# Kernel tuning notes

Measured on AMD Instinct MI355X. Metric: run time of the kernel, lower is better.

The kernel has to match this reference:

```python
import jax, jax.numpy as jnp
import numpy as np

NEG = -1e12


def setup_inputs() -> dict:
    key = jax.random.key(0)
    ks = jax.random.split(key, 6)
    B, S, D, H = 32, 2048, 1024, 1024  # batch, seq, dec/enc dim, hidden
    last_state = jax.random.normal(ks[0], (B, D), dtype=jnp.float32)
    enc_outputs = jax.random.normal(ks[1], (B, S, D), dtype=jnp.float32)
    attn_masks = jax.random.randint(ks[2], (B, S), 0, 2, dtype=jnp.int32)
    W = jax.random.normal(ks[3], (H, 2 * D), dtype=jnp.float32) * 0.02
    b = jax.random.normal(ks[4], (H,), dtype=jnp.float32) * 0.02
    V = jax.random.normal(ks[5], (H,), dtype=jnp.float32)
    return {"last_state": last_state, "enc_outputs": enc_outputs,
            "attn_masks": attn_masks, "W": W, "b": b, "V": V}


def reference(last_state, enc_outputs, attn_masks, W, b, V):
    # Split W to avoid materializing the [B,S,2D] concat:
    # concat([h, e]) @ W.T == h @ Wh.T + e @ We.T
    D = last_state.shape[-1]
    Wh, We = W[:, :D], W[:, D:]
    # hidden part: [B,H], broadcast over seq
    h_part = jnp.einsum('bd,hd->bh', last_state, Wh)  # [B,H]
    e_part = jnp.einsum('bsd,hd->bsh', enc_outputs, We)  # [B,S,H]
    sim = jnp.tanh(h_part[:, None, :] + e_part + b)  # [B,S,H]
    scores = jnp.einsum('bsh,h->bs', sim, V)  # [B,S]
    scores = jnp.where(attn_masks != 1, jnp.float32(NEG), scores)
    attn_weights = jax.nn.softmax(scores, axis=1)  # [B,S]
    context = jnp.einsum('bs,bsd->bd', attn_weights, enc_outputs)  # [B,D]
    return context, attn_weights, scores
```

## Files before the change

### kernel.cpp

```cpp
#include <hip/hip_runtime.h>
#include <math.h>
#include <stdint.h>

#define B_ 32
#define S_ 2048
#define D_ 1024
#define H_ 1024
#define NEGV -1000000000000.0f

typedef __attribute__((ext_vector_type(8))) short bf16x8;
typedef __attribute__((ext_vector_type(8))) _Float16 f16x8;
typedef __attribute__((ext_vector_type(4))) float f32x4;

static __device__ __forceinline__ unsigned short f2bf(float x) {
    union { float f; unsigned u; } v; v.f = x;
    unsigned r = v.u + 0x7FFF + ((v.u >> 16) & 1);
    return (unsigned short)(r >> 16);
}
static __device__ __forceinline__ float bf2f(unsigned short h) {
    union { float f; unsigned u; } v; v.u = ((unsigned)h) << 16; return v.f;
}
static __device__ __forceinline__ unsigned short f2h(float x) {
    _Float16 h = (_Float16)x; unsigned short u;
    __builtin_memcpy(&u, &h, 2); return u;
}
static __device__ __forceinline__ float h2f(unsigned short u) {
    _Float16 h; __builtin_memcpy(&h, &u, 2); return (float)h;
}
static __device__ __forceinline__ float tanh_fast(float x) {
    float e = __expf(2.f * x);
    return 1.f - 2.f / (e + 1.f);
}
static __device__ __forceinline__ void gl_lds16(unsigned short* lds, const unsigned short* g) {
    __builtin_amdgcn_global_load_lds(
        (const __attribute__((address_space(1))) unsigned int*)(const void*)g,
        (__attribute__((address_space(3))) unsigned int*)(void*)lds,
        16, 0, 0);
}

__global__ __launch_bounds__(256) void k_W_f16(const float* __restrict__ W,
                                               unsigned short* __restrict__ out) {
    int idx = blockIdx.x * 256 + threadIdx.x;
    int h = idx >> 7, kc = idx & 127;
    const float* src = W + (size_t)h * (2 * D_) + D_ + kc * 8;
    float4 a = *(const float4*)src;
    float4 c4 = *(const float4*)(src + 4);
    float v[8] = {a.x, a.y, a.z, a.w, c4.x, c4.y, c4.z, c4.w};
    unsigned short t[8];
#pragma unroll
    for (int j = 0; j < 8; ++j) t[j] = f2h(v[j]);
    uint4 w;
    w.x = t[0] | ((unsigned)t[1] << 16); w.y = t[2] | ((unsigned)t[3] << 16);
    w.z = t[4] | ((unsigned)t[5] << 16); w.w = t[6] | ((unsigned)t[7] << 16);
    int g = kc >> 3, cc = kc & 7;
    int dst = g * 64 + ((cc ^ (h & 7)) << 3);
    *(uint4*)(out + (size_t)h * D_ + dst) = w;
}

__global__ __launch_bounds__(256) void k_hpart(const float* __restrict__ ls,
                                               const float* __restrict__ W,
                                               float* __restrict__ hp) {
    int bh = blockIdx.x * 256 + threadIdx.x;
    int b = bh >> 10, h = bh & 1023;
    const float* lsr = ls + b * D_;
    const float* wr  = W + (size_t)h * (2 * D_);
    float acc = 0.f;
#pragma unroll 4
    for (int d = 0; d < D_; d += 4) {
        float4 a = *(const float4*)(lsr + d);
        float4 w = *(const float4*)(wr + d);
        acc += a.x * w.x + a.y * w.y + a.z * w.z + a.w * w.w;
    }
    hp[bh] = acc;
}

__global__ __launch_bounds__(512, 2) void k_scores_fused(
    const float* __restrict__ enc,
    const unsigned short* __restrict__ Wf16,
    const float* __restrict__ hp, const float* __restrict__ bias,
    const float* __restrict__ V, float* __restrict__ spart)
{
    extern __shared__ unsigned short smem[];
    unsigned short* smemA = smem;
    unsigned short* smemB = smem + 16384;

    const int tid  = threadIdx.x;
    const int lane = tid & 63, wid = tid >> 6;
    const int wm = wid >> 2, wn = wid & 3;
    const int l15 = lane & 15, lhi = lane >> 4;

    const int bid  = blockIdx.x;
    const int wgid = (bid & 7) * 128 + (bid >> 3);
    const int mt = wgid >> 2, nt = wgid & 3;
    const int m0 = mt * 256;
    const int nt256 = nt * 256;
    const int b = m0 >> 11;

    const size_t boff = (size_t)(nt256 + wid * 16 + (lane >> 3)) * D_ + (lane & 7) * 8;
    const int ldsw = wid * 1024;

    f32x4 acc[8][4];
#pragma unroll
    for (int i = 0; i < 8; ++i)
#pragma unroll
        for (int j = 0; j < 4; ++j)
            acc[i][j] = (f32x4){0.f, 0.f, 0.f, 0.f};

    const int swz = l15 & 7;

    float4 ar0[4], ar1[4];

#define LOAD_A(KOFS) do {                                                           \
    _Pragma("unroll")                                                               \
    for (int s_ = 0; s_ < 4; ++s_) {                                                \
        int p_ = tid + s_ * 512;                                                    \
        int row_ = p_ >> 3, pc_ = p_ & 7;                                           \
        const float* ap_ = enc + (size_t)(m0 + row_) * D_ + (KOFS) + pc_ * 8;       \
        ar0[s_] = *(const float4*)ap_;                                              \
        ar1[s_] = *(const float4*)(ap_ + 4);                                        \
    }                                                                               \
} while (0)
#define WRITE_A() do {                                                              \
    _Pragma("unroll")                                                               \
    for (int s_ = 0; s_ < 4; ++s_) {                                                \
        int p_ = tid + s_ * 512;                                                    \
        int row_ = p_ >> 3, pc_ = p_ & 7;                                           \
        float v_[8] = {ar0[s_].x, ar0[s_].y, ar0[s_].z, ar0[s_].w,                  \
                       ar1[s_].x, ar1[s_].y, ar1[s_].z, ar1[s_].w};                 \
        unsigned short t_[8];                                                       \
        _Pragma("unroll")                                                           \
        for (int j_ = 0; j_ < 8; ++j_) t_[j_] = f2h(v_[j_]);                        \
        uint4 w_;                                                                   \
        w_.x = t_[0] | ((unsigned)t_[1] << 16); w_.y = t_[2] | ((unsigned)t_[3] << 16); \
        w_.z = t_[4] | ((unsigned)t_[5] << 16); w_.w = t_[6] | ((unsigned)t_[7] << 16); \
        *(uint4*)&smemA[row_ * 64 + ((pc_ ^ (row_ & 7)) << 3)] = w_;                \
    }                                                                               \
} while (0)

#define STAGE_B(HALF, KOFS) do {                                                    \
    unsigned short* d_ = &smemB[(HALF) * 8192 + ldsw];                              \
    const unsigned short* s_ = Wf16 + boff + (size_t)(HALF) * 131072 + (KOFS);      \
    gl_lds16(d_, s_);                                                               \
    gl_lds16(d_ + 512, s_ + 8192);                                                  \
} while (0)

#define LDA(AR, MH, KS) do {                                                        \
    _Pragma("unroll")                                                               \
    for (int fi_ = 0; fi_ < 4; ++fi_) {                                             \
        int row_ = wm * 128 + (MH) * 64 + fi_ * 16 + l15;                           \
        int ch_  = ((KS) * 4 + lhi) ^ swz;                                          \
        AR[fi_] = *(const f16x8*)&smemA[row_ * 64 + ch_ * 8];                       \
    }                                                                               \
} while (0)
#define LDB(BR, KS) do {                                                            \
    _Pragma("unroll")                                                               \
    for (int fi_ = 0; fi_ < 4; ++fi_) {                                             \
        int row_ = wn * 64 + fi_ * 16 + l15;                                        \
        int ch_  = ((KS) * 4 + lhi) ^ swz;                                          \
        BR[fi_] = *(const f16x8*)&smemB[row_ * 64 + ch_ * 8];                       \
    }                                                                               \
} while (0)
#define MFMA16(AR, BR, MH) do {                                                     \
    _Pragma("unroll")                                                               \
    for (int fi_ = 0; fi_ < 4; ++fi_)                                               \
    _Pragma("unroll")                                                               \
        for (int fj_ = 0; fj_ < 4; ++fj_)                                           \
            acc[(MH) * 4 + fi_][fj_] = __builtin_amdgcn_mfma_f32_16x16x32_f16(      \
                AR[fi_], BR[fj_], acc[(MH) * 4 + fi_][fj_], 0, 0, 0);               \
} while (0)

    LOAD_A(0);
    WRITE_A();
    STAGE_B(0, 0);
    STAGE_B(1, 0);
    __syncthreads();

    f16x8 a[4], bk[4];
#pragma unroll 1
    for (int t = 0; t < 16; ++t) {
        const int kofs = (t + 1) * 64;

        if (t < 15) LOAD_A(kofs);

#pragma unroll
        for (int ks = 0; ks < 2; ++ks) {
            LDB(bk, ks);
            LDA(a, 0, ks);
            MFMA16(a, bk, 0);
            LDA(a, 1, ks);
            MFMA16(a, bk, 1);
        }

        __syncthreads();

        if (t < 15) {
            WRITE_A();
            STAGE_B(0, kofs);
            STAGE_B(1, kofs);
        }

        __syncthreads();
    }

    float hb[4], vv[4];
#pragma unroll
    for (int fn = 0; fn < 4; ++fn) {
        int h = nt256 + wn * 64 + fn * 16 + l15;
        hb[fn] = hp[b * H_ + h] + bias[h];
        vv[fn] = V[h];
    }
    float* s_red = (float*)smem;
#pragma unroll
    for (int fm = 0; fm < 8; ++fm)
#pragma unroll
        for (int rg = 0; rg < 4; ++rg) {
            float rs = 0.f;
#pragma unroll
            for (int fn = 0; fn < 4; ++fn)
                rs += tanh_fast(acc[fm][fn][rg] + hb[fn]) * vv[fn];
            rs += __shfl_xor(rs, 1, 16);
            rs += __shfl_xor(rs, 2, 16);
            rs += __shfl_xor(rs, 4, 16);
            rs += __shfl_xor(rs, 8, 16);
            if (l15 == 0)
                s_red[wid * 128 + fm * 16 + lhi * 4 + rg] = rs;
        }
    __syncthreads();
    if (tid < 256) {
        int wmr = tid >> 7, rr = tid & 127;
        float v = s_red[(wmr * 4 + 0) * 128 + rr] + s_red[(wmr * 4 + 1) * 128 + rr]
                + s_red[(wmr * 4 + 2) * 128 + rr] + s_red[(wmr * 4 + 3) * 128 + rr];
        spart[(size_t)nt * 65536 + m0 + tid] = v;
    }
#undef LOAD_A
#undef WRITE_A
#undef STAGE_B
#undef LDA
#undef LDB
#undef MFMA16
}

__global__ __launch_bounds__(256) void k_softmax_fold(const float* __restrict__ spart,
                                                      const int* __restrict__ mask,
                                                      float* __restrict__ scores_out,
                                                      float* __restrict__ weights) {
    __shared__ float red[8];
    int b = blockIdx.x, tid = threadIdx.x;
    float vals[8];
    float mx = -INFINITY;
#pragma unroll
    for (int i = 0; i < 8; ++i) {
        int m = b * S_ + tid + i * 256;
        float s = spart[m] + spart[65536 + m] + spart[131072 + m] + spart[196608 + m];
        s = (mask[m] == 1) ? s : NEGV;
        scores_out[m] = s;
        vals[i] = s;
        mx = fmaxf(mx, s);
    }
    for (int off = 32; off; off >>= 1) mx = fmaxf(mx, __shfl_xor(mx, off, 64));
    int wave = tid >> 6;
    if ((tid & 63) == 0) red[wave] = mx;
    __syncthreads();
    mx = fmaxf(fmaxf(red[0], red[1]), fmaxf(red[2], red[3]));
    float sum = 0.f;
#pragma unroll
    for (int i = 0; i < 8; ++i) {
        vals[i] = expf(vals[i] - mx);
        sum += vals[i];
    }
    for (int off = 32; off; off >>= 1) sum += __shfl_xor(sum, off, 64);
    if ((tid & 63) == 0) red[4 + wave] = sum;
    __syncthreads();
    sum = red[4] + red[5] + red[6] + red[7];
    float inv = 1.f / sum;
#pragma unroll
    for (int i = 0; i < 8; ++i)
        weights[b * S_ + tid + i * 256] = vals[i] * inv;
}

__global__ __launch_bounds__(256) void k_ctx_partial_f32(const float* __restrict__ weights,
                                                         const float* __restrict__ enc,
                                                         float* __restrict__ part) {
    int b = blockIdx.x >> 4;
    int chunk = blockIdx.x & 15;
    int tid = threadIdx.x;
    int d0 = tid * 4;
    float4 acc = {0.f, 0.f, 0.f, 0.f};
    int s0 = chunk * 128;
    const float* wrow = weights + b * S_;
    for (int s = s0; s < s0 + 128; ++s) {
        float w = wrow[s];
        if (w != 0.f) {
            float4 e = *(const float4*)(enc + (size_t)(b * S_ + s) * D_ + d0);
            acc.x += w * e.x; acc.y += w * e.y; acc.z += w * e.z; acc.w += w * e.w;
        }
    }
    *(float4*)(part + (size_t)blockIdx.x * D_ + d0) = acc;
}

__global__ __launch_bounds__(256) void k_ctx_reduce(const float* __restrict__ part,
                                                    float* __restrict__ ctx) {
    int bd = blockIdx.x * 256 + threadIdx.x;
    int b = bd >> 10, d = bd & 1023;
    float acc = 0.f;
#pragma unroll
    for (int c = 0; c < 16; ++c)
        acc += part[(size_t)(b * 16 + c) * D_ + d];
    ctx[bd] = acc;
}

__global__ __launch_bounds__(256) void k_splitW_lin(const float* __restrict__ W,
                                                    unsigned short* __restrict__ hi,
                                                    unsigned short* __restrict__ lo) {
    int idx = blockIdx.x * 256 + threadIdx.x;
    int h = idx >> 7, kc = idx & 127;
    const float* src = W + (size_t)h * (2 * D_) + D_ + kc * 8;
    float4 a = *(const float4*)src;
    float4 c = *(const float4*)(src + 4);
    float v[8] = {a.x, a.y, a.z, a.w, c.x, c.y, c.z, c.w};
    unsigned short th[8], tl[8];
#pragma unroll
    for (int j = 0; j < 8; ++j) {
        th[j] = f2bf(v[j]);
        tl[j] = f2bf(v[j] - bf2f(th[j]));
    }
    uint4 hw, lw;
    hw.x = th[0] | ((unsigned)th[1] << 16); hw.y = th[2] | ((unsigned)th[3] << 16);
    hw.z = th[4] | ((unsigned)th[5] << 16); hw.w = th[6] | ((unsigned)th[7] << 16);
    lw.x = tl[0] | ((unsigned)tl[1] << 16); lw.y = tl[2] | ((unsigned)tl[3] << 16);
    lw.z = tl[4] | ((unsigned)tl[5] << 16); lw.w = tl[6] | ((unsigned)tl[7] << 16);
    *(uint4*)(hi + (size_t)h * D_ + kc * 8) = hw;
    *(uint4*)(lo + (size_t)h * D_ + kc * 8) = lw;
}

__global__ __launch_bounds__(256, 2) void k_scores_mfma_fb(
    const float* __restrict__ enc,
    const unsigned short* __restrict__ Whi,
    const unsigned short* __restrict__ Wlo,
    const float* __restrict__ hp,
    const float* __restrict__ bias,
    const float* __restrict__ V,
    const int* __restrict__ mask,
    float* __restrict__ scores_out)
{
    __shared__ __align__(16) unsigned short smem[4 * 8192];
    unsigned short* sAhi = smem;
    unsigned short* sAlo = smem + 8192;
    unsigned short* sBhi = smem + 16384;
    unsigned short* sBlo = smem + 24576;

    const int tid  = threadIdx.x;
    const int lane = tid & 63, wid = tid >> 6;
    const int wr = wid >> 1, wc = wid & 1;
    const int l15 = lane & 15, lhi = lane >> 4;
    const int m0 = blockIdx.x * 128;
    const int b  = m0 >> 11;

    float rowsum[4][4] = {};
    float4 pa[8];
    uint4  pbh[4], pbl[4];

#define STAGE_LOAD(NB, KB) do {                                            \
    _Pragma("unroll")                                                      \
    for (int i_ = 0; i_ < 4; ++i_) {                                       \
        int c_ = tid + i_ * 256;                                           \
        int r_ = c_ >> 3, kc_ = c_ & 7;                                    \
        const float* ap_ = enc + (size_t)(m0 + r_) * D_ + (KB) * 64 + kc_ * 8; \
        pa[2 * i_]     = *(const float4*)ap_;                              \
        pa[2 * i_ + 1] = *(const float4*)(ap_ + 4);                        \
        size_t bo_ = (size_t)((NB) * 128 + r_) * D_ + (KB) * 64 + kc_ * 8; \
        pbh[i_] = *(const uint4*)(Whi + bo_);                              \
        pbl[i_] = *(const uint4*)(Wlo + bo_);                              \
    }                                                                      \
} while (0)

#define STAGE_WRITE() do {                                                 \
    _Pragma("unroll")                                                      \
    for (int i_ = 0; i_ < 4; ++i_) {                                       \
        int c_ = tid + i_ * 256;                                           \
        int sc_ = c_ ^ ((c_ >> 3) & 7);                                    \
        float vv_[8] = {pa[2*i_].x, pa[2*i_].y, pa[2*i_].z, pa[2*i_].w,    \
                        pa[2*i_+1].x, pa[2*i_+1].y, pa[2*i_+1].z, pa[2*i_+1].w}; \
        unsigned short th_[8], tl_[8];                                     \
        _Pragma("unroll")                                                  \
        for (int j_ = 0; j_ < 8; ++j_) {                                   \
            th_[j_] = f2bf(vv_[j_]);                                       \
            tl_[j_] = f2bf(vv_[j_] - bf2f(th_[j_]));                       \
        }                                                                  \
        uint4 hw_, lw_;                                                    \
        hw_.x = th_[0] | ((unsigned)th_[1] << 16); hw_.y = th_[2] | ((unsigned)th_[3] << 16); \
        hw_.z = th_[4] | ((unsigned)th_[5] << 16); hw_.w = th_[6] | ((unsigned)th_[7] << 16); \
        lw_.x = tl_[0] | ((unsigned)tl_[1] << 16); lw_.y = tl_[2] | ((unsigned)tl_[3] << 16); \
        lw_.z = tl_[4] | ((unsigned)tl_[5] << 16); lw_.w = tl_[6] | ((unsigned)tl_[7] << 16); \
        *(uint4*)&sAhi[sc_ * 8] = hw_;                                     \
        *(uint4*)&sAlo[sc_ * 8] = lw_;                                     \
        *(uint4*)&sBhi[sc_ * 8] = pbh[i_];                                 \
        *(uint4*)&sBlo[sc_ * 8] = pbl[i_];                                 \
    }                                                                      \
} while (0)

    STAGE_LOAD(0, 0);

    for (int nb = 0; nb < 8; ++nb) {
        f32x4 acc[4][4];
#pragma unroll
        for (int i = 0; i < 4; ++i)
#pragma unroll
            for (int j = 0; j < 4; ++j)
                acc[i][j] = (f32x4){0.f, 0.f, 0.f, 0.f};

        for (int kb = 0; kb < 16; ++kb) {
            __syncthreads();
            STAGE_WRITE();
            __syncthreads();
            int nkb = kb + 1, nnb = nb;
            if (nkb == 16) { nkb = 0; nnb = nb + 1; }
            if (nnb < 8) STAGE_LOAD(nnb, nkb);

#pragma unroll
            for (int ks = 0; ks < 2; ++ks) {
                bf16x8 bh[4], bl[4];
#pragma unroll
                for (int fn = 0; fn < 4; ++fn) {
                    int rB = wc * 64 + fn * 16 + l15;
                    int ch = (rB * 8 + ks * 4 + lhi) ^ (rB & 7);
                    bh[fn] = *(const bf16x8*)&sBhi[ch * 8];
                    bl[fn] = *(const bf16x8*)&sBlo[ch * 8];
                }
#pragma unroll
                for (int fm = 0; fm < 4; ++fm) {
                    int rA = wr * 64 + fm * 16 + l15;
                    int ch = (rA * 8 + ks * 4 + lhi) ^ (rA & 7);
                    bf16x8 ah = *(const bf16x8*)&sAhi[ch * 8];
                    bf16x8 al = *(const bf16x8*)&sAlo[ch * 8];
#pragma unroll
                    for (int fn = 0; fn < 4; ++fn) {
                        acc[fm][fn] = __builtin_amdgcn_mfma_f32_16x16x32_bf16(ah, bh[fn], acc[fm][fn], 0, 0, 0);
                        acc[fm][fn] = __builtin_amdgcn_mfma_f32_16x16x32_bf16(ah, bl[fn], acc[fm][fn], 0, 0, 0);
                        acc[fm][fn] = __builtin_amdgcn_mfma_f32_16x16x32_bf16(al, bh[fn], acc[fm][fn], 0, 0, 0);
                    }
                }
            }
        }

        int n0 = nb * 128;
#pragma unroll
        for (int fn = 0; fn < 4; ++fn) {
            int n = n0 + wc * 64 + fn * 16 + l15;
            float hbv = hp[b * H_ + n] + bias[n];
            float vvv = V[n];
#pragma unroll
            for (int fm = 0; fm < 4; ++fm) {
                f32x4 a = acc[fm][fn];
#pragma unroll
                for (int rg = 0; rg < 4; ++rg)
                    rowsum[fm][rg] += tanh_fast(a[rg] + hbv) * vvv;
            }
        }
    }

    __syncthreads();
    float* s_red = (float*)smem;
#pragma unroll
    for (int fm = 0; fm < 4; ++fm)
#pragma unroll
        for (int rg = 0; rg < 4; ++rg) {
            float v = rowsum[fm][rg];
            v += __shfl_xor(v, 1, 16);
            v += __shfl_xor(v, 2, 16);
            v += __shfl_xor(v, 4, 16);
            v += __shfl_xor(v, 8, 16);
            if (l15 == 0)
                s_red[wc * 128 + wr * 64 + fm * 16 + lhi * 4 + rg] = v;
        }
    __syncthreads();
    if (tid < 128) {
        int m = m0 + tid;
        float sc = s_red[tid] + s_red[128 + tid];
        scores_out[m] = (mask[m] == 1) ? sc : NEGV;
    }
#undef STAGE_LOAD
#undef STAGE_WRITE
}

__global__ __launch_bounds__(256) void k_softmax(const float* __restrict__ scores,
                                                 float* __restrict__ weights) {
    __shared__ float red[8];
    int b = blockIdx.x;
    int tid = threadIdx.x;
    const float* srow = scores + b * S_;
    float vals[8];
    float mx = -INFINITY;
#pragma unroll
    for (int i = 0; i < 8; ++i) {
        vals[i] = srow[tid + i * 256];
        mx = fmaxf(mx, vals[i]);
    }
    for (int off = 32; off; off >>= 1) mx = fmaxf(mx, __shfl_xor(mx, off, 64));
    int wave = tid >> 6;
    if ((tid & 63) == 0) red[wave] = mx;
    __syncthreads();
    mx = fmaxf(fmaxf(red[0], red[1]), fmaxf(red[2], red[3]));
    float sum = 0.f;
#pragma unroll
    for (int i = 0; i < 8; ++i) {
        vals[i] = expf(vals[i] - mx);
        sum += vals[i];
    }
    for (int off = 32; off; off >>= 1) sum += __shfl_xor(sum, off, 64);
    if ((tid & 63) == 0) red[4 + wave] = sum;
    __syncthreads();
    sum = red[4] + red[5] + red[6] + red[7];
    float inv = 1.f / sum;
#pragma unroll
    for (int i = 0; i < 8; ++i)
        weights[b * S_ + tid + i * 256] = vals[i] * inv;
}

extern "C" void kernel_launch(void* const* d_in, const int* in_sizes, int n_in,
                              void* d_out, int out_size, void* d_ws, size_t ws_size,
                              hipStream_t stream) {
    const float* ls   = (const float*)d_in[0];
    const float* enc  = (const float*)d_in[1];
    const int*   mask = (const int*)d_in[2];
    const float* W    = (const float*)d_in[3];
    const float* bias = (const float*)d_in[4];
    const float* V    = (const float*)d_in[5];

    float* out     = (float*)d_out;
    float* ctx     = out;
    float* weights = out + 32768;
    float* scores  = out + 98304;

    const size_t need = 2097152ull + 131072ull + 1048576ull + 2097152ull;

    if (ws_size >= need) {
        unsigned short* Wf16 = (unsigned short*)d_ws;
        float* hp    = (float*)(Wf16 + 1048576);
        float* spart = hp + 32768;
        float* part  = spart + 262144;

        hipFuncSetAttribute((const void*)k_scores_fused,
                            hipFuncAttributeMaxDynamicSharedMemorySize, 65536);

        k_W_f16<<<512, 256, 0, stream>>>(W, Wf16);
        k_hpart<<<128, 256, 0, stream>>>(ls, W, hp);
        k_scores_fused<<<1024, 512, 65536, stream>>>(enc, Wf16, hp, bias, V, spart);
        k_softmax_fold<<<32, 256, 0, stream>>>(spart, mask, scores, weights);
        k_ctx_partial_f32<<<512, 256, 0, stream>>>(weights, enc, part);
        k_ctx_reduce<<<128, 256, 0, stream>>>(part, ctx);
    } else {
        unsigned short* Whi = (unsigned short*)d_ws;
        unsigned short* Wlo = Whi + 1048576;
        float* hp   = (float*)(Wlo + 1048576);
        float* part = hp + 32768;

        k_splitW_lin<<<512, 256, 0, stream>>>(W, Whi, Wlo);
        k_hpart<<<128, 256, 0, stream>>>(ls, W, hp);
        k_scores_mfma_fb<<<512, 256, 0, stream>>>(enc, Whi, Wlo, hp, bias, V, mask, scores);
        k_softmax<<<32, 256, 0, stream>>>(scores, weights);
        k_ctx_partial_f32<<<512, 256, 0, stream>>>(weights, enc, part);
        k_ctx_reduce<<<128, 256, 0, stream>>>(part, ctx);
    }
}
```

Baseline: 262.7 us.

## Shrink scores GEMM M-tile to 128 and widen K-step to 128

Retiles the fused score GEMM so each block covers 128 sequence rows by 256 hidden units, and stages 128 K columns per step instead of 64. This halves the number of K-loop iterations and barriers. It doubles the grid to 2048 blocks, and the f16 weight layout and LDS XOR swizzle are widened to 16 chunks to match. The cost is that dynamic LDS per block grows to 96KB, which likely drops resident blocks per CU from two to one. Each block also now reuses a staged B tile over half as many rows, so more weight traffic is needed in total.

```diff
diff --git a/kernel.cpp b/kernel.cpp
--- a/kernel.cpp
+++ b/kernel.cpp
@@ -52,8 +52,8 @@
     uint4 w;
     w.x = t[0] | ((unsigned)t[1] << 16); w.y = t[2] | ((unsigned)t[3] << 16);
     w.z = t[4] | ((unsigned)t[5] << 16); w.w = t[6] | ((unsigned)t[7] << 16);
-    int g = kc >> 3, cc = kc & 7;
-    int dst = g * 64 + ((cc ^ (h & 7)) << 3);
+    int g = kc >> 4, cc = kc & 15;
+    int dst = g * 128 + ((cc ^ (h & 15)) << 3);
     *(uint4*)(out + (size_t)h * D_ + dst) = w;
 }
 
@@ -74,7 +74,7 @@
     hp[bh] = acc;
 }
 
-__global__ __launch_bounds__(512, 2) void k_scores_fused(
+__global__ __launch_bounds__(512, 2) void k_scores_m128(
     const float* __restrict__ enc,
     const unsigned short* __restrict__ Wf16,
     const float* __restrict__ hp, const float* __restrict__ bias,
@@ -90,23 +90,23 @@
     const int l15 = lane & 15, lhi = lane >> 4;
 
     const int bid  = blockIdx.x;
-    const int wgid = (bid & 7) * 128 + (bid >> 3);
+    const int wgid = (bid & 7) * 256 + (bid >> 3);
     const int mt = wgid >> 2, nt = wgid & 3;
-    const int m0 = mt * 256;
+    const int m0 = mt * 128;
     const int nt256 = nt * 256;
     const int b = m0 >> 11;
 
-    const size_t boff = (size_t)(nt256 + wid * 16 + (lane >> 3)) * D_ + (lane & 7) * 8;
-    const int ldsw = wid * 1024;
-
-    f32x4 acc[8][4];
-#pragma unroll
-    for (int i = 0; i < 8; ++i)
+    const size_t boff = (size_t)(nt256 + wid * 32 + (lane >> 4)) * D_ + (lane & 15) * 8;
+    const int ldsb = wid * 4096;
+
+    f32x4 acc[4][4];
+#pragma unroll
+    for (int i = 0; i < 4; ++i)
 #pragma unroll
         for (int j = 0; j < 4; ++j)
             acc[i][j] = (f32x4){0.f, 0.f, 0.f, 0.f};
 
-    const int swz = l15 & 7;
+    const int swz = l15;
 
     float4 ar0[4], ar1[4];
 
@@ -114,7 +114,7 @@
     _Pragma("unroll")                                                               \
     for (int s_ = 0; s_ < 4; ++s_) {                                                \
         int p_ = tid + s_ * 512;                                                    \
-        int row_ = p_ >> 3, pc_ = p_ & 7;                                           \
+        int row_ = p_ >> 4, pc_ = p_ & 15;                                          \
         const float* ap_ = enc + (size_t)(m0 + row_) * D_ + (KOFS) + pc_ * 8;       \
         ar0[s_] = *(const float4*)ap_;                                              \
         ar1[s_] = *(const float4*)(ap_ + 4);                                        \
@@ -124,7 +124,7 @@
     _Pragma("unroll")                                                               \
     for (int s_ = 0; s_ < 4; ++s_) {                                                \
         int p_ = tid + s_ * 512;                                                    \
-        int row_ = p_ >> 3, pc_ = p_ & 7;                                           \
+        int row_ = p_ >> 4, pc_ = p_ & 15;                                          \
         float v_[8] = {ar0[s_].x, ar0[s_].y, ar0[s_].z, ar0[s_].w,                  \
                        ar1[s_].x, ar1[s_].y, ar1[s_].z, ar1[s_].w};                 \
         unsigned short t_[8];                                                       \
@@ -133,23 +133,22 @@
         uint4 w_;                                                                   \
         w_.x = t_[0] | ((unsigned)t_[1] << 16); w_.y = t_[2] | ((unsigned)t_[3] << 16); \
         w_.z = t_[4] | ((unsigned)t_[5] << 16); w_.w = t_[6] | ((unsigned)t_[7] << 16); \
-        *(uint4*)&smemA[row_ * 64 + ((pc_ ^ (row_ & 7)) << 3)] = w_;                \
+        *(uint4*)&smemA[row_ * 128 + ((pc_ ^ (row_ & 15)) << 3)] = w_;              \
     }                                                                               \
 } while (0)
 
-#define STAGE_B(HALF, KOFS) do {                                                    \
-    unsigned short* d_ = &smemB[(HALF) * 8192 + ldsw];                              \
-    const unsigned short* s_ = Wf16 + boff + (size_t)(HALF) * 131072 + (KOFS);      \
-    gl_lds16(d_, s_);                                                               \
-    gl_lds16(d_ + 512, s_ + 8192);                                                  \
-} while (0)
-
-#define LDA(AR, MH, KS) do {                                                        \
+#define STAGE_B(KOFS) do {                                                          \
+    _Pragma("unroll")                                                               \
+    for (int j_ = 0; j_ < 8; ++j_)                                                  \
+        gl_lds16(&smemB[ldsb + j_ * 512], Wf16 + boff + (size_t)j_ * 4 * D_ + (KOFS)); \
+} while (0)
+
+#define LDA(AR, KS) do {                                                            \
     _Pragma("unroll")                                                               \
     for (int fi_ = 0; fi_ < 4; ++fi_) {                                             \
-        int row_ = wm * 128 + (MH) * 64 + fi_ * 16 + l15;                           \
+        int row_ = wm * 64 + fi_ * 16 + l15;                                        \
         int ch_  = ((KS) * 4 + lhi) ^ swz;                                          \
-        AR[fi_] = *(const f16x8*)&smemA[row_ * 64 + ch_ * 8];                       \
+        AR[fi_] = *(const f16x8*)&smemA[row_ * 128 + ch_ * 8];                      \
     }                                                                               \
 } while (0)
 #define LDB(BR, KS) do {                                                            \
@@ -157,46 +156,42 @@
     for (int fi_ = 0; fi_ < 4; ++fi_) {                                             \
         int row_ = wn * 64 + fi_ * 16 + l15;                                        \
         int ch_  = ((KS) * 4 + lhi) ^ swz;                                          \
-        BR[fi_] = *(const f16x8*)&smemB[row_ * 64 + ch_ * 8];                       \
+        BR[fi_] = *(const f16x8*)&smemB[row_ * 128 + ch_ * 8];                      \
     }                                                                               \
 } while (0)
-#define MFMA16(AR, BR, MH) do {                                                     \
+#define MFMA16(AR, BR) do {                                                         \
     _Pragma("unroll")                                                               \
     for (int fi_ = 0; fi_ < 4; ++fi_)                                               \
     _Pragma("unroll")                                                               \
         for (int fj_ = 0; fj_ < 4; ++fj_)                                           \
-            acc[(MH) * 4 + fi_][fj_] = __builtin_amdgcn_mfma_f32_16x16x32_f16(      \
-                AR[fi_], BR[fj_], acc[(MH) * 4 + fi_][fj_], 0, 0, 0);               \
+            acc[fi_][fj_] = __builtin_amdgcn_mfma_f32_16x16x32_f16(                 \
+                AR[fi_], BR[fj_], acc[fi_][fj_], 0, 0, 0);                          \
 } while (0)
 
     LOAD_A(0);
     WRITE_A();
-    STAGE_B(0, 0);
-    STAGE_B(1, 0);
+    STAGE_B(0);
     __syncthreads();
 
     f16x8 a[4], bk[4];
 #pragma unroll 1
-    for (int t = 0; t < 16; ++t) {
-        const int kofs = (t + 1) * 64;
-
-        if (t < 15) LOAD_A(kofs);
-
-#pragma unroll
-        for (int ks = 0; ks < 2; ++ks) {
+    for (int t = 0; t < 8; ++t) {
+        const int kofs = (t + 1) * 128;
+
+        if (t < 7) LOAD_A(kofs);
+
+#pragma unroll
+        for (int ks = 0; ks < 4; ++ks) {
             LDB(bk, ks);
-            LDA(a, 0, ks);
-            MFMA16(a, bk, 0);
-            LDA(a, 1, ks);
-            MFMA16(a, bk, 1);
+            LDA(a, ks);
+            MFMA16(a, bk);
         }
 
         __syncthreads();
 
-        if (t < 15) {
+        if (t < 7) {
             WRITE_A();
-            STAGE_B(0, kofs);
-            STAGE_B(1, kofs);
+            STAGE_B(kofs);
         }
 
         __syncthreads();
@@ -211,7 +206,7 @@
     }
     float* s_red = (float*)smem;
 #pragma unroll
-    for (int fm = 0; fm < 8; ++fm)
+    for (int fm = 0; fm < 4; ++fm)
 #pragma unroll
         for (int rg = 0; rg < 4; ++rg) {
             float rs = 0.f;
@@ -223,13 +218,11 @@
             rs += __shfl_xor(rs, 4, 16);
             rs += __shfl_xor(rs, 8, 16);
             if (l15 == 0)
-                s_red[wid * 128 + fm * 16 + lhi * 4 + rg] = rs;
-        }
-    __syncthreads();
-    if (tid < 256) {
-        int wmr = tid >> 7, rr = tid & 127;
-        float v = s_red[(wmr * 4 + 0) * 128 + rr] + s_red[(wmr * 4 + 1) * 128 + rr]
-                + s_red[(wmr * 4 + 2) * 128 + rr] + s_red[(wmr * 4 + 3) * 128 + rr];
+                s_red[wn * 128 + wm * 64 + fm * 16 + lhi * 4 + rg] = rs;
+        }
+    __syncthreads();
+    if (tid < 128) {
+        float v = s_red[tid] + s_red[128 + tid] + s_red[256 + tid] + s_red[384 + tid];
         spart[(size_t)nt * 65536 + m0 + tid] = v;
     }
 #undef LOAD_A
@@ -540,12 +533,12 @@
         float* spart = hp + 32768;
         float* part  = spart + 262144;
 
-        hipFuncSetAttribute((const void*)k_scores_fused,
-                            hipFuncAttributeMaxDynamicSharedMemorySize, 65536);
+        hipFuncSetAttribute((const void*)k_scores_m128,
+                            hipFuncAttributeMaxDynamicSharedMemorySize, 98304);
 
         k_W_f16<<<512, 256, 0, stream>>>(W, Wf16);
         k_hpart<<<128, 256, 0, stream>>>(ls, W, hp);
-        k_scores_fused<<<1024, 512, 65536, stream>>>(enc, Wf16, hp, bias, V, spart);
+        k_scores_m128<<<2048, 512, 98304, stream>>>(enc, Wf16, hp, bias, V, spart);
         k_softmax_fold<<<32, 256, 0, stream>>>(spart, mask, scores, weights);
         k_ctx_partial_f32<<<512, 256, 0, stream>>>(weights, enc, part);
         k_ctx_reduce<<<128, 256, 0, stream>>>(part, ctx);
```

After: 288.1 us. 9.7% more time.
